# Kernel optimization log

Measured on AMD Instinct MI355X. Metric: run time of the kernel, lower is better.

The kernel has to match this reference:

```python
import jax, jax.numpy as jnp
import numpy as np

N_USERS = 100000
N_ITEMS = 50000
N_NODES = N_USERS + N_ITEMS
LATENT = 64
NNZ = 2400000
BATCH = 2048
EPS = 1e-12  # F.normalize eps


def setup_inputs() -> dict:
    key = jax.random.key(0)
    ks = jax.random.split(key, 16)
    inp = {
        "rows": jax.random.randint(ks[0], (NNZ,), 0, N_NODES, dtype=jnp.int32),
        "cols": jax.random.randint(ks[1], (NNZ,), 0, N_NODES, dtype=jnp.int32),
        "vals": jax.random.uniform(ks[2], (NNZ,), dtype=jnp.float32),
        "x": jax.random.normal(ks[3], (N_NODES, LATENT), dtype=jnp.float32) * 0.1,
        "users": jax.random.randint(ks[12], (BATCH,), 0, N_USERS, dtype=jnp.int32),
        "items": jax.random.randint(ks[13], (BATCH,), 0, N_ITEMS, dtype=jnp.int32),
    }
    for k in range(2):
        inp[f"W_gc{k}"] = jax.random.normal(ks[4 + 4 * k], (LATENT, LATENT), dtype=jnp.float32) * 0.1
        inp[f"b_gc{k}"] = jax.random.normal(ks[5 + 4 * k], (1, LATENT), dtype=jnp.float32) * 0.1
        inp[f"W_bi{k}"] = jax.random.normal(ks[6 + 4 * k], (LATENT, LATENT), dtype=jnp.float32) * 0.1
        inp[f"b_bi{k}"] = jax.random.normal(ks[7 + 4 * k], (1, LATENT), dtype=jnp.float32) * 0.1
    return inp


def _l2_normalize(v):
    # F.normalize(p=2, dim=1): divide by max(||v||_2, eps)
    n = jnp.sqrt(jnp.sum(v * v, axis=1, keepdims=True))
    return v / jnp.maximum(n, EPS)


def reference(rows, cols, vals, x,
              W_gc0, b_gc0, W_bi0, b_bi0,
              W_gc1, b_gc1, W_bi1, b_bi1,
              users, items):
    weights = [(W_gc0, b_gc0, W_bi0, b_bi0), (W_gc1, b_gc1, W_bi1, b_bi1)]
    ego = x                      # [N, D]
    embs = [x]
    for (Wg, bg, Wb, bb) in weights:
        # sparse adj @ ego  (COO gather + segment-sum scatter)
        msgs = vals[:, None] * ego[cols]                              # [nnz, D]
        side = jax.ops.segment_sum(msgs, rows, num_segments=N_NODES)  # [N, D]
        sum_emb = side @ Wg + bg
        bi_emb = (ego * side) @ Wb + bb
        ego = _l2_normalize(jax.nn.leaky_relu(sum_emb + bi_emb, negative_slope=0.2))
        embs.append(ego)
    all_emb = jnp.concatenate(embs, axis=1)          # [N, 3*D]
    users_emb = all_emb[users]                       # [B, 3*D]
    items_emb = all_emb[N_USERS + items]             # [B, 3*D]
    gamma = jnp.sum(users_emb * items_emb, axis=1)   # [B]
    return gamma
```

## Files before the change

kernel.cpp:

```cpp
#include <hip/hip_runtime.h>

#define N_USERS_C 100000
#define N_NODES_C 150000
#define D 64
#define NB 2344
#define NSUP 74
#define CPAD 16
#define SPAD 68
#define FCAP 1536
#define SCAP 36864
#define S1CAP 2352
#define S2CAP 2560
#define BPS 16

__global__ __launch_bounds__(256) void mark1_k(
    const int* __restrict__ u, const int* __restrict__ it,
    unsigned char* __restrict__ samp, unsigned char* __restrict__ need, int batch)
{
    int i = blockIdx.x * blockDim.x + threadIdx.x;
    if (i >= 2 * batch) return;
    int n = (i < batch) ? u[i] : N_USERS_C + it[i - batch];
    samp[n] = 1;
    need[n] = 1;
}

__global__ __launch_bounds__(256) void mark2_k(
    const int* __restrict__ rows, const int* __restrict__ cols,
    const unsigned char* __restrict__ samp, unsigned char* __restrict__ need, int nnz)
{
    int gtid = blockIdx.x * blockDim.x + threadIdx.x;
    int stride = gridDim.x * blockDim.x;
    for (int e = gtid; e < nnz; e += stride)
        if (samp[rows[e]]) need[cols[e]] = 1;
}

__global__ __launch_bounds__(1024) void scan1_k(
    const unsigned char* __restrict__ need, int* __restrict__ part,
    int* __restrict__ bsum, int n)
{
    __shared__ int wsum[16];
    int i = blockIdx.x * 1024 + threadIdx.x;
    int lane = threadIdx.x & 63, wid = threadIdx.x >> 6;
    int v = (i < n) ? (int)need[i] : 0;
    int incl = v;
    #pragma unroll
    for (int off = 1; off < 64; off <<= 1) {
        int t = __shfl_up(incl, off);
        if (lane >= off) incl += t;
    }
    if (lane == 63) wsum[wid] = incl;
    __syncthreads();
    int woff = 0;
    for (int w = 0; w < wid; ++w) woff += wsum[w];
    if (i < n) part[i] = woff + incl - v;
    if (threadIdx.x == 1023) bsum[blockIdx.x] = woff + incl;
}

__global__ __launch_bounds__(1024) void scan2_k(
    int* __restrict__ bsum, int nb, int* __restrict__ Mptr)
{
    __shared__ int wsum[16];
    int lane = threadIdx.x & 63, wid = threadIdx.x >> 6;
    int i = threadIdx.x;
    int v = (i < nb) ? bsum[i] : 0;
    int incl = v;
    #pragma unroll
    for (int off = 1; off < 64; off <<= 1) {
        int t = __shfl_up(incl, off);
        if (lane >= off) incl += t;
    }
    if (lane == 63) wsum[wid] = incl;
    __syncthreads();
    int woff = 0;
    for (int w = 0; w < wid; ++w) woff += wsum[w];
    if (i < nb) bsum[i] = woff + incl - v;
    if (i == nb - 1) Mptr[0] = woff + incl;
}

__global__ __launch_bounds__(256) void scan3_k(
    const int* __restrict__ bsum, int* __restrict__ idx,
    const unsigned char* __restrict__ need, int* __restrict__ list, int n)
{
    int i = blockIdx.x * blockDim.x + threadIdx.x;
    if (i >= n) return;
    int t = idx[i] + bsum[i >> 10];
    if (need[i]) { idx[i] = t; list[t] = i; }
    else idx[i] = -1;
}

__global__ __launch_bounds__(256) void initcur_k(
    int* __restrict__ bcur, int* __restrict__ scur)
{
    int i = blockIdx.x * blockDim.x + threadIdx.x;
    if (i < NB) bcur[i * CPAD] = i * FCAP;
    if (i < NSUP) scur[i * CPAD] = i * SCAP;
}

__global__ __launch_bounds__(256) void s1_k(
    const int* __restrict__ rows, const int* __restrict__ cols,
    const float* __restrict__ vals, const int* __restrict__ idx,
    int* __restrict__ scurP, int2* __restrict__ pairs1, int nnz)
{
    __shared__ int2 sbuf[S1CAP];
    __shared__ unsigned char smap[S1CAP];
    __shared__ int lcnt[NSUP], lofs[NSUP], lcur[NSUP], gb[NSUP];
    __shared__ int stot;
    int t = threadIdx.x;
    for (int i = t; i < NSUP; i += 256) lcnt[i] = 0;
    __syncthreads();
    int per = (nnz + gridDim.x - 1) / gridDim.x;
    int s = blockIdx.x * per;
    int e = min(nnz, s + per);
    for (int i = s + t; i < e; i += 256) {
        int ci = idx[rows[i]];
        if (ci >= 0) atomicAdd(&lcnt[ci >> 11], 1);
    }
    __syncthreads();
    if (t == 0) {
        int run = 0;
        for (int i = 0; i < NSUP; ++i) { lofs[i] = run; run += lcnt[i]; }
        stot = run;
    }
    __syncthreads();
    for (int i = t; i < NSUP; i += 256) {
        int c = lcnt[i];
        gb[i] = c ? atomicAdd(&scurP[i * CPAD], c) : 0;
        lcur[i] = lofs[i];
    }
    __syncthreads();
    for (int i = s + t; i < e; i += 256) {
        int ci = idx[rows[i]];
        if (ci < 0) continue;
        int sp = ci >> 11;
        int dst = atomicAdd(&lcur[sp], 1);
        sbuf[dst] = make_int2(((ci & 2047) << 18) | cols[i], __float_as_int(vals[i]));
        smap[dst] = (unsigned char)sp;
    }
    __syncthreads();
    int m = stot;
    for (int i = t; i < m; i += 256) {
        int sp = smap[i];
        pairs1[gb[sp] + (i - lofs[sp])] = sbuf[i];
    }
}

__global__ __launch_bounds__(256) void s2_k(
    const int* __restrict__ scurP, const int2* __restrict__ pairs1,
    int* __restrict__ bcurP, int2* __restrict__ pairs)
{
    __shared__ int2 sbuf[S2CAP];
    __shared__ unsigned char fmap[S2CAP];
    __shared__ int fcnt[32], fofs[32], fcur[32], gb[32];
    int sp = blockIdx.x / BPS, part = blockIdx.x % BPS;
    int lo = sp * SCAP, hi = scurP[sp * CPAD];
    int len = hi - lo;
    if (len <= 0) return;
    int per = (len + BPS - 1) / BPS;
    int cs = lo + part * per;
    int ce = min(hi, cs + per);
    int m = ce - cs;
    if (m <= 0) return;
    int t = threadIdx.x;
    if (t < 32) fcnt[t] = 0;
    __syncthreads();
    for (int i = t; i < m; i += 256)
        atomicAdd(&fcnt[(pairs1[cs + i].x >> 18) >> 6], 1);
    __syncthreads();
    if (t < 32) {
        int v = fcnt[t], incl = v;
        #pragma unroll
        for (int o = 1; o < 32; o <<= 1) {
            int u = __shfl_up(incl, o);
            if (t >= o) incl += u;
        }
        fofs[t] = incl - v;
        fcur[t] = incl - v;
        gb[t] = v ? atomicAdd(&bcurP[(sp * 32 + t) * CPAD], v) : 0;
    }
    __syncthreads();
    for (int i = t; i < m; i += 256) {
        int2 p = pairs1[cs + i];
        int ris = p.x >> 18;
        int f = ris >> 6;
        int dst = atomicAdd(&fcur[f], 1);
        sbuf[dst] = make_int2(((ris & 63) << 18) | (p.x & 0x3FFFF), p.y);
        fmap[dst] = (unsigned char)f;
    }
    __syncthreads();
    for (int i = t; i < m; i += 256) {
        int f = fmap[i];
        pairs[gb[f] + (i - fofs[f])] = sbuf[i];
    }
}

__global__ __launch_bounds__(256) void sortb_k(
    const int* __restrict__ bcurP, int2* __restrict__ pairs,
    int* __restrict__ rp)
{
    __shared__ int2 buf[FCAP];
    __shared__ int cnt[64];
    __shared__ int cur[64];
    int b = blockIdx.x;
    int s = b * FCAP;
    int e = bcurP[b * CPAD];
    int m = e - s;
    int t = threadIdx.x;
    if (t < 64) cnt[t] = 0;
    __syncthreads();
    for (int i = t; i < m; i += 256) {
        int2 p = pairs[s + i];
        buf[i] = p;
        atomicAdd(&cnt[p.x >> 18], 1);
    }
    __syncthreads();
    if (t < 64) {
        int v = cnt[t];
        int incl = v;
        #pragma unroll
        for (int o = 1; o < 64; o <<= 1) {
            int u = __shfl_up(incl, o);
            if (t >= o) incl += u;
        }
        cur[t] = incl - v;
        rp[b * 65 + t] = s + incl - v;
        if (t == 63) rp[b * 65 + 64] = s + incl;
    }
    __syncthreads();
    for (int i = t; i < m; i += 256) {
        int2 p = buf[i];
        int dst = atomicAdd(&cur[p.x >> 18], 1);
        pairs[s + dst] = make_int2(p.x & 0x3FFFF, p.y);
    }
}

__global__ __launch_bounds__(256) void gather1_k(
    const int* __restrict__ rp, const int2* __restrict__ pairs,
    const float* __restrict__ x, float* __restrict__ side,
    const int* __restrict__ Mptr)
{
    int gtid = blockIdx.x * blockDim.x + threadIdx.x;
    int wave = gtid >> 6;
    int lane = threadIdx.x & 63;
    if (wave >= Mptr[0]) return;
    int rb = (wave >> 6) * 65 + (wave & 63);
    int s  = rp[rb];
    int ep = rp[rb + 1];

    float acc = 0.0f;
    for (int base = s; base < ep; base += 64) {
        int2 p = make_int2(0, 0);
        if (base + lane < ep) p = pairs[base + lane];
        int cnt4 = (min(ep - base, 64) + 3) & ~3;
        for (int j = 0; j < cnt4; j += 4) {
            int c0 = __shfl(p.x, j + 0);
            int c1 = __shfl(p.x, j + 1);
            int c2 = __shfl(p.x, j + 2);
            int c3 = __shfl(p.x, j + 3);
            float v0 = __int_as_float(__shfl(p.y, j + 0));
            float v1 = __int_as_float(__shfl(p.y, j + 1));
            float v2 = __int_as_float(__shfl(p.y, j + 2));
            float v3 = __int_as_float(__shfl(p.y, j + 3));
            float f0 = x[(size_t)c0 * D + lane];
            float f1 = x[(size_t)c1 * D + lane];
            float f2 = x[(size_t)c2 * D + lane];
            float f3 = x[(size_t)c3 * D + lane];
            acc = fmaf(v0, f0, acc);
            acc = fmaf(v1, f1, acc);
            acc = fmaf(v2, f2, acc);
            acc = fmaf(v3, f3, acc);
        }
    }
    side[(size_t)wave * D + lane] = acc;
}

__global__ __launch_bounds__(256) void gather2_k(
    const int* __restrict__ rp, const int2* __restrict__ pairs,
    const float* __restrict__ e1c, const int* __restrict__ idx,
    float* __restrict__ side2c, float* __restrict__ egoc,
    const int* __restrict__ u, const int* __restrict__ it, int batch)
{
    int gtid = blockIdx.x * blockDim.x + threadIdx.x;
    int wave = gtid >> 6;
    int lane = threadIdx.x & 63;
    if (wave >= 2 * batch) return;
    int n = (wave < batch) ? u[wave] : N_USERS_C + it[wave - batch];
    int cr = idx[n];
    int rb = (cr >> 6) * 65 + (cr & 63);
    int s  = rp[rb];
    int ep = rp[rb + 1];

    float acc = 0.0f;
    for (int base = s; base < ep; base += 64) {
        int2 p = make_int2(0, 0);
        if (base + lane < ep) p = pairs[base + lane];
        int cnt = min(ep - base, 64);
        for (int j = 0; j < cnt; ++j) {
            int   c = __shfl(p.x, j);
            float v = __int_as_float(__shfl(p.y, j));
            acc = fmaf(v, e1c[(size_t)idx[c] * D + lane], acc);
        }
    }
    side2c[(size_t)wave * D + lane] = acc;
    egoc[(size_t)wave * D + lane] = e1c[(size_t)cr * D + lane];
}

__global__ __launch_bounds__(256) void transform_k(
    const float* __restrict__ S, const float* __restrict__ Eb,
    const float* __restrict__ Wg, const float* __restrict__ bg,
    const float* __restrict__ Wb, const float* __restrict__ bb,
    float* __restrict__ out, const int* __restrict__ list,
    const int* __restrict__ Mptr, int nrows)
{
    __shared__ __align__(16) float sWg[D * D];
    __shared__ __align__(16) float sWb[D * D];
    __shared__ __align__(16) float sAT[D][SPAD];
    __shared__ __align__(16) float sBT[D][SPAD];

    int nr = Mptr ? Mptr[0] : nrows;
    int t  = threadIdx.x;
    int tc = t & 15;
    int tr = t >> 4;
    int r0 = blockIdx.x * 64;
    if (r0 >= nr) return;

    for (int i = t; i < D * D; i += 256) {
        sWg[i] = Wg[i];
        sWb[i] = Wb[i];
    }
    for (int itr = 0; itr < 4; ++itr) {
        int rr  = itr * 16 + (t >> 4);
        int row = r0 + rr;
        float4 sv = make_float4(0.f, 0.f, 0.f, 0.f);
        float4 ev = sv;
        if (row < nr) {
            sv = *(const float4*)&S[(size_t)row * D + tc * 4];
            int er = list ? list[row] : row;
            ev = *(const float4*)&Eb[(size_t)er * D + tc * 4];
        }
        sAT[tc * 4 + 0][rr] = sv.x;
        sAT[tc * 4 + 1][rr] = sv.y;
        sAT[tc * 4 + 2][rr] = sv.z;
        sAT[tc * 4 + 3][rr] = sv.w;
        sBT[tc * 4 + 0][rr] = sv.x * ev.x;
        sBT[tc * 4 + 1][rr] = sv.y * ev.y;
        sBT[tc * 4 + 2][rr] = sv.z * ev.z;
        sBT[tc * 4 + 3][rr] = sv.w * ev.w;
    }
    __syncthreads();

    float acc[4][4] = {};
    for (int k = 0; k < D; ++k) {
        float4 a4 = *(const float4*)&sAT[k][tr * 4];
        float4 b4 = *(const float4*)&sBT[k][tr * 4];
        float4 g4 = *(const float4*)&sWg[k * D + tc * 4];
        float4 w4 = *(const float4*)&sWb[k * D + tc * 4];
        float av[4] = {a4.x, a4.y, a4.z, a4.w};
        float bv[4] = {b4.x, b4.y, b4.z, b4.w};
        float gv[4] = {g4.x, g4.y, g4.z, g4.w};
        float wv[4] = {w4.x, w4.y, w4.z, w4.w};
        #pragma unroll
        for (int i = 0; i < 4; ++i)
            #pragma unroll
            for (int j = 0; j < 4; ++j)
                acc[i][j] = fmaf(av[i], gv[j], fmaf(bv[i], wv[j], acc[i][j]));
    }

    float4 bgv = *(const float4*)&bg[tc * 4];
    float4 bbv = *(const float4*)&bb[tc * 4];
    float bias[4] = {bgv.x + bbv.x, bgv.y + bbv.y, bgv.z + bbv.z, bgv.w + bbv.w};

    float vv[4][4];
    float ss[4] = {0.f, 0.f, 0.f, 0.f};
    #pragma unroll
    for (int i = 0; i < 4; ++i) {
        #pragma unroll
        for (int j = 0; j < 4; ++j) {
            float v = acc[i][j] + bias[j];
            v = (v > 0.0f) ? v : 0.2f * v;
            vv[i][j] = v;
            ss[i] += v * v;
        }
    }
    #pragma unroll
    for (int i = 0; i < 4; ++i) {
        #pragma unroll
        for (int off = 1; off < 16; off <<= 1)
            ss[i] += __shfl_xor(ss[i], off);
    }
    #pragma unroll
    for (int i = 0; i < 4; ++i) {
        int row = r0 + tr * 4 + i;
        if (row < nr) {
            float inv = 1.0f / fmaxf(sqrtf(ss[i]), 1e-12f);
            float4 o = make_float4(vv[i][0] * inv, vv[i][1] * inv,
                                   vv[i][2] * inv, vv[i][3] * inv);
            *(float4*)&out[(size_t)row * D + tc * 4] = o;
        }
    }
}

__global__ __launch_bounds__(256) void gamma_k(
    const float* __restrict__ x, const float* __restrict__ e1c,
    const int* __restrict__ idx, const float* __restrict__ e2c,
    const int* __restrict__ users, const int* __restrict__ items,
    float* __restrict__ gamma, int batch)
{
    int gtid = blockIdx.x * blockDim.x + threadIdx.x;
    int wave = gtid >> 6;
    int lane = threadIdx.x & 63;
    if (wave >= batch) return;
    size_t uu = (size_t)users[wave];
    size_t tt = (size_t)(N_USERS_C + items[wave]);
    float acc = x[uu * D + lane] * x[tt * D + lane]
              + e1c[(size_t)idx[uu] * D + lane] * e1c[(size_t)idx[tt] * D + lane]
              + e2c[(size_t)wave * D + lane] * e2c[(size_t)(batch + wave) * D + lane];
    #pragma unroll
    for (int off = 1; off < 64; off <<= 1) acc += __shfl_xor(acc, off);
    if (lane == 0) gamma[wave] = acc;
}

extern "C" void kernel_launch(void* const* d_in, const int* in_sizes, int n_in,
                              void* d_out, int out_size, void* d_ws, size_t ws_size,
                              hipStream_t stream) {
    const int*   rows  = (const int*)d_in[0];
    const int*   cols  = (const int*)d_in[1];
    const float* vals  = (const float*)d_in[2];
    const float* x     = (const float*)d_in[3];
    const int*   users = (const int*)d_in[4];
    const int*   items = (const int*)d_in[5];
    const float* Wg0 = (const float*)d_in[6];
    const float* bg0 = (const float*)d_in[7];
    const float* Wb0 = (const float*)d_in[8];
    const float* bb0 = (const float*)d_in[9];
    const float* Wg1 = (const float*)d_in[10];
    const float* bg1 = (const float*)d_in[11];
    const float* Wb1 = (const float*)d_in[12];
    const float* bb1 = (const float*)d_in[13];

    int nnz   = in_sizes[0];
    int batch = in_sizes[4];
    float* out = (float*)d_out;

    size_t emb = (size_t)N_NODES_C * D;
    float* A      = (float*)d_ws;
    float* Sbuf   = A + emb;
    int*   bcur   = (int*)(Sbuf + emb);
    int*   scur   = bcur + NB * CPAD;
    int*   rp     = scur + NSUP * CPAD;
    int*   idx    = rp + NB * 65 + 2;
    int*   list   = idx + N_NODES_C;
    int*   bsum   = list + N_NODES_C;
    int*   Mptr   = bsum + 1024;
    unsigned char* need = (unsigned char*)(Mptr + 4);
    unsigned char* samp = need + N_NODES_C;
    int2*  pairs  = (int2*)(((size_t)(samp + N_NODES_C) + 15) & ~(size_t)15);

    int2*  pairs1 = (int2*)Sbuf;
    float* side2c = Sbuf;
    float* egoc   = Sbuf + (size_t)2 * 2048 * D;
    float* e2c    = egoc + (size_t)2 * 2048 * D;

    int nscan = (N_NODES_C + 1023) / 1024;

    hipMemsetAsync(need, 0, 2 * N_NODES_C, stream);
    mark1_k<<<(2 * batch + 255) / 256, 256, 0, stream>>>(users, items, samp, need, batch);
    mark2_k<<<1024, 256, 0, stream>>>(rows, cols, samp, need, nnz);
    scan1_k<<<nscan, 1024, 0, stream>>>(need, idx, bsum, N_NODES_C);
    scan2_k<<<1, 1024, 0, stream>>>(bsum, nscan, Mptr);
    scan3_k<<<(N_NODES_C + 255) / 256, 256, 0, stream>>>(bsum, idx, need, list, N_NODES_C);

    initcur_k<<<(NB + 255) / 256, 256, 0, stream>>>(bcur, scur);
    int g1 = (nnz + 2343) / 2344;
    s1_k<<<g1, 256, 0, stream>>>(rows, cols, vals, idx, scur, pairs1, nnz);
    s2_k<<<NSUP * BPS, 256, 0, stream>>>(scur, pairs1, bcur, pairs);
    sortb_k<<<NB, 256, 0, stream>>>(bcur, pairs, rp);

    gather1_k<<<(N_NODES_C * 64 + 255) / 256, 256, 0, stream>>>(
        rp, pairs, x, Sbuf, Mptr);
    transform_k<<<(N_NODES_C + 63) / 64, 256, 0, stream>>>(
        Sbuf, x, Wg0, bg0, Wb0, bb0, A, list, Mptr, 0);

    gather2_k<<<(2 * batch * 64 + 255) / 256, 256, 0, stream>>>(
        rp, pairs, A, idx, side2c, egoc, users, items, batch);
    transform_k<<<(2 * batch + 63) / 64, 256, 0, stream>>>(
        side2c, egoc, Wg1, bg1, Wb1, bb1, e2c, nullptr, nullptr, 2 * batch);

    gamma_k<<<(batch * 64 + 255) / 256, 256, 0, stream>>>(
        x, A, idx, e2c, users, items, out, batch);
}
```

Baseline: 296.5 us.

## Replace global-atomic super-bucket scatter with fixed per-block fragments

The first bucketing pass now uses 256 blocks of 512 threads. Each block writes its pairs straight into a fixed-size fragment per super-bucket and records the count in a count table, so the block-local staging, prefix scan and global atomic cursors go away. The second pass reads its 16 fragments per super-bucket into shared memory, counts and scatters into fine buckets. This cuts passes over the edges and global atomics, but drops the coalesced write-out and relies on each fragment staying within 240 entries and each s2 block's total within 2560, which random inputs should satisfy.

```diff
diff --git a/kernel.cpp b/kernel.cpp
--- a/kernel.cpp
+++ b/kernel.cpp
@@ -8,10 +8,11 @@
 #define CPAD 16
 #define SPAD 68
 #define FCAP 1536
-#define SCAP 36864
-#define S1CAP 2352
+#define S1B 256
+#define FRAG 240
 #define S2CAP 2560
 #define BPS 16
+#define FPB (S1B / BPS)
 
 __global__ __launch_bounds__(256) void mark1_k(
     const int* __restrict__ u, const int* __restrict__ it,
@@ -88,108 +89,71 @@
     else idx[i] = -1;
 }
 
-__global__ __launch_bounds__(256) void initcur_k(
-    int* __restrict__ bcur, int* __restrict__ scur)
+__global__ __launch_bounds__(256) void initcur_k(int* __restrict__ bcur)
 {
     int i = blockIdx.x * blockDim.x + threadIdx.x;
     if (i < NB) bcur[i * CPAD] = i * FCAP;
-    if (i < NSUP) scur[i * CPAD] = i * SCAP;
-}
-
-__global__ __launch_bounds__(256) void s1_k(
+}
+
+__global__ __launch_bounds__(512) void s1_k(
     const int* __restrict__ rows, const int* __restrict__ cols,
     const float* __restrict__ vals, const int* __restrict__ idx,
-    int* __restrict__ scurP, int2* __restrict__ pairs1, int nnz)
-{
-    __shared__ int2 sbuf[S1CAP];
-    __shared__ unsigned char smap[S1CAP];
-    __shared__ int lcnt[NSUP], lofs[NSUP], lcur[NSUP], gb[NSUP];
-    __shared__ int stot;
+    int2* __restrict__ pairs1, int* __restrict__ scnt, int nnz)
+{
+    __shared__ int lcur[NSUP];
     int t = threadIdx.x;
-    for (int i = t; i < NSUP; i += 256) lcnt[i] = 0;
-    __syncthreads();
-    int per = (nnz + gridDim.x - 1) / gridDim.x;
-    int s = blockIdx.x * per;
+    for (int i = t; i < NSUP; i += 512) lcur[i] = 0;
+    __syncthreads();
+    int b = blockIdx.x;
+    int per = (nnz + S1B - 1) / S1B;
+    int s = b * per;
     int e = min(nnz, s + per);
-    for (int i = s + t; i < e; i += 256) {
-        int ci = idx[rows[i]];
-        if (ci >= 0) atomicAdd(&lcnt[ci >> 11], 1);
-    }
-    __syncthreads();
-    if (t == 0) {
-        int run = 0;
-        for (int i = 0; i < NSUP; ++i) { lofs[i] = run; run += lcnt[i]; }
-        stot = run;
-    }
-    __syncthreads();
-    for (int i = t; i < NSUP; i += 256) {
-        int c = lcnt[i];
-        gb[i] = c ? atomicAdd(&scurP[i * CPAD], c) : 0;
-        lcur[i] = lofs[i];
-    }
-    __syncthreads();
-    for (int i = s + t; i < e; i += 256) {
+    for (int i = s + t; i < e; i += 512) {
         int ci = idx[rows[i]];
         if (ci < 0) continue;
         int sp = ci >> 11;
-        int dst = atomicAdd(&lcur[sp], 1);
-        sbuf[dst] = make_int2(((ci & 2047) << 18) | cols[i], __float_as_int(vals[i]));
-        smap[dst] = (unsigned char)sp;
-    }
-    __syncthreads();
-    int m = stot;
-    for (int i = t; i < m; i += 256) {
-        int sp = smap[i];
-        pairs1[gb[sp] + (i - lofs[sp])] = sbuf[i];
-    }
+        int k = atomicAdd(&lcur[sp], 1);
+        pairs1[(size_t)sp * (S1B * FRAG) + b * FRAG + k] =
+            make_int2(((ci & 2047) << 18) | cols[i], __float_as_int(vals[i]));
+    }
+    __syncthreads();
+    for (int i = t; i < NSUP; i += 512) scnt[i * S1B + b] = lcur[i];
 }
 
 __global__ __launch_bounds__(256) void s2_k(
-    const int* __restrict__ scurP, const int2* __restrict__ pairs1,
+    const int* __restrict__ scnt, const int2* __restrict__ pairs1,
     int* __restrict__ bcurP, int2* __restrict__ pairs)
 {
     __shared__ int2 sbuf[S2CAP];
-    __shared__ unsigned char fmap[S2CAP];
-    __shared__ int fcnt[32], fofs[32], fcur[32], gb[32];
+    __shared__ int fcnt[32], fcur[32], gb[32];
     int sp = blockIdx.x / BPS, part = blockIdx.x % BPS;
-    int lo = sp * SCAP, hi = scurP[sp * CPAD];
-    int len = hi - lo;
-    if (len <= 0) return;
-    int per = (len + BPS - 1) / BPS;
-    int cs = lo + part * per;
-    int ce = min(hi, cs + per);
-    int m = ce - cs;
-    if (m <= 0) return;
     int t = threadIdx.x;
-    if (t < 32) fcnt[t] = 0;
-    __syncthreads();
-    for (int i = t; i < m; i += 256)
-        atomicAdd(&fcnt[(pairs1[cs + i].x >> 18) >> 6], 1);
+    if (t < 32) { fcnt[t] = 0; fcur[t] = 0; }
+    __syncthreads();
+    int base = 0;
+    for (int fi = 0; fi < FPB; ++fi) {
+        int b = part * FPB + fi;
+        int m = scnt[sp * S1B + b];
+        const int2* src = &pairs1[(size_t)sp * (S1B * FRAG) + b * FRAG];
+        for (int i = t; i < m; i += 256) {
+            int2 p = src[i];
+            sbuf[base + i] = p;
+            atomicAdd(&fcnt[(p.x >> 18) >> 6], 1);
+        }
+        base += m;
+    }
     __syncthreads();
     if (t < 32) {
-        int v = fcnt[t], incl = v;
-        #pragma unroll
-        for (int o = 1; o < 32; o <<= 1) {
-            int u = __shfl_up(incl, o);
-            if (t >= o) incl += u;
-        }
-        fofs[t] = incl - v;
-        fcur[t] = incl - v;
-        gb[t] = v ? atomicAdd(&bcurP[(sp * 32 + t) * CPAD], v) : 0;
-    }
-    __syncthreads();
-    for (int i = t; i < m; i += 256) {
-        int2 p = pairs1[cs + i];
+        int c = fcnt[t];
+        gb[t] = c ? atomicAdd(&bcurP[(sp * 32 + t) * CPAD], c) : 0;
+    }
+    __syncthreads();
+    for (int i = t; i < base; i += 256) {
+        int2 p = sbuf[i];
         int ris = p.x >> 18;
         int f = ris >> 6;
-        int dst = atomicAdd(&fcur[f], 1);
-        sbuf[dst] = make_int2(((ris & 63) << 18) | (p.x & 0x3FFFF), p.y);
-        fmap[dst] = (unsigned char)f;
-    }
-    __syncthreads();
-    for (int i = t; i < m; i += 256) {
-        int f = fmap[i];
-        pairs[gb[f] + (i - fofs[f])] = sbuf[i];
+        int k = atomicAdd(&fcur[f], 1);
+        pairs[gb[f] + k] = make_int2(((ris & 63) << 18) | (p.x & 0x3FFFF), p.y);
     }
 }
 
@@ -445,13 +409,13 @@
     float* A      = (float*)d_ws;
     float* Sbuf   = A + emb;
     int*   bcur   = (int*)(Sbuf + emb);
-    int*   scur   = bcur + NB * CPAD;
-    int*   rp     = scur + NSUP * CPAD;
+    int*   rp     = bcur + NB * CPAD;
     int*   idx    = rp + NB * 65 + 2;
     int*   list   = idx + N_NODES_C;
     int*   bsum   = list + N_NODES_C;
     int*   Mptr   = bsum + 1024;
-    unsigned char* need = (unsigned char*)(Mptr + 4);
+    int*   scnt   = Mptr + 4;
+    unsigned char* need = (unsigned char*)(scnt + NSUP * S1B);
     unsigned char* samp = need + N_NODES_C;
     int2*  pairs  = (int2*)(((size_t)(samp + N_NODES_C) + 15) & ~(size_t)15);
 
@@ -469,10 +433,9 @@
     scan2_k<<<1, 1024, 0, stream>>>(bsum, nscan, Mptr);
     scan3_k<<<(N_NODES_C + 255) / 256, 256, 0, stream>>>(bsum, idx, need, list, N_NODES_C);
 
-    initcur_k<<<(NB + 255) / 256, 256, 0, stream>>>(bcur, scur);
-    int g1 = (nnz + 2343) / 2344;
-    s1_k<<<g1, 256, 0, stream>>>(rows, cols, vals, idx, scur, pairs1, nnz);
-    s2_k<<<NSUP * BPS, 256, 0, stream>>>(scur, pairs1, bcur, pairs);
+    initcur_k<<<(NB + 255) / 256, 256, 0, stream>>>(bcur);
+    s1_k<<<S1B, 512, 0, stream>>>(rows, cols, vals, idx, pairs1, scnt, nnz);
+    s2_k<<<NSUP * BPS, 256, 0, stream>>>(scnt, pairs1, bcur, pairs);
     sortb_k<<<NB, 256, 0, stream>>>(bcur, pairs, rp);
 
     gather1_k<<<(N_NODES_C * 64 + 255) / 256, 256, 0, stream>>>(
```

Result: faster. 275.9 us (-7.0%).
